# Kernel tuning notes

Hardware: AMD Instinct MI355X
Metric: run time of the kernel (lower is better)

Reference implementation:

```python
import jax, jax.numpy as jnp
import numpy as np

D_MODEL = 1024
NUM_HEADS = 16
D_K = D_MODEL // NUM_HEADS


def setup_inputs() -> dict:
    key = jax.random.key(0)
    ks = jax.random.split(key, 9)
    s = 1.0 / np.sqrt(D_MODEL)
    x = jax.random.normal(ks[0], (4, 2048, D_MODEL), dtype=jnp.float32)
    wq = jax.random.uniform(ks[1], (D_MODEL, D_MODEL), jnp.float32, -s, s)
    bq = jax.random.uniform(ks[2], (D_MODEL,), jnp.float32, -s, s)
    wk = jax.random.uniform(ks[3], (D_MODEL, D_MODEL), jnp.float32, -s, s)
    bk = jax.random.uniform(ks[4], (D_MODEL,), jnp.float32, -s, s)
    wv = jax.random.uniform(ks[5], (D_MODEL, D_MODEL), jnp.float32, -s, s)
    bv = jax.random.uniform(ks[6], (D_MODEL,), jnp.float32, -s, s)
    wo = jax.random.uniform(ks[7], (D_MODEL, D_MODEL), jnp.float32, -s, s)
    bo = jax.random.uniform(ks[8], (D_MODEL,), jnp.float32, -s, s)
    return {"x": x, "wq": wq, "bq": bq, "wk": wk, "bk": bk,
            "wv": wv, "bv": bv, "wo": wo, "bo": bo}


def reference(x, wq, bq, wk, bk, wv, bv, wo, bo):
    B, S, _ = x.shape
    H, Dk = NUM_HEADS, D_K
    # QKV projections (torch Linear: y = x @ W.T + b; here w* stored as [in,out])
    q = (x @ wq + bq).reshape(B, S, H, Dk).transpose(0, 2, 1, 3)  # [B,H,S,Dk]
    k = (x @ wk + bk).reshape(B, S, H, Dk).transpose(0, 2, 1, 3)
    v = (x @ wv + bv).reshape(B, S, H, Dk).transpose(0, 2, 1, 3)
    scores = jnp.einsum('bhqd,bhkd->bhqk', q, k) / jnp.sqrt(jnp.float32(Dk))
    attn = jax.nn.softmax(scores, axis=-1)
    out = jnp.einsum('bhqk,bhkd->bhqd', attn, v)  # [B,H,S,Dk]
    out = out.transpose(0, 2, 1, 3).reshape(B, S, H * Dk)
    return out @ wo + bo
```

## Files before the change

### kernel.cpp

```cpp
#include <hip/hip_runtime.h>
#include <hip/hip_bf16.h>
#include <cstdint>

#define D_MODEL 1024
#define NHEAD 16
#define DKH 64
#define BATCH 4
#define SEQ 2048
#define M_TOT (BATCH*SEQ)

typedef __bf16 bf16;
typedef __bf16 bf16x8 __attribute__((ext_vector_type(8)));
typedef __bf16 bf16x4 __attribute__((ext_vector_type(4)));
typedef float  f32x4  __attribute__((ext_vector_type(4)));

__device__ __forceinline__ void async_ld16(const void* g, void* l) {
    __builtin_amdgcn_global_load_lds(
        (__attribute__((address_space(1))) void*)(uintptr_t)g,
        (__attribute__((address_space(3))) void*)(uintptr_t)l,
        16, 0, 0);
}

__global__ __launch_bounds__(256) void k_cvt(const float* __restrict__ x,
                                             bf16* __restrict__ xb,
                                             const float* __restrict__ wq,
                                             const float* __restrict__ wk,
                                             const float* __restrict__ wv,
                                             const float* __restrict__ wo,
                                             bf16* __restrict__ wt) {
    __shared__ float t[32][33];
    int bid = blockIdx.x;
    if (bid < 8192) {
        int i = (bid * 256 + threadIdx.x) * 4;
        float4 f = *(const float4*)(x + i);
        bf16x4 o;
        o[0] = (bf16)f.x; o[1] = (bf16)f.y; o[2] = (bf16)f.z; o[3] = (bf16)f.w;
        *(bf16x4*)(xb + i) = o;
    } else {
        int wb = bid - 8192;
        int z = wb >> 10;
        int rem = wb & 1023;
        const float* W = (z == 0) ? wq : (z == 1) ? wk : (z == 2) ? wv : wo;
        bf16* T = wt + (size_t)z * D_MODEL * D_MODEL;
        int tx = threadIdx.x & 31, ty = threadIdx.x >> 5;
        int bx = (rem & 31) * 32, by = (rem >> 5) * 32;
#pragma unroll
        for (int i = 0; i < 4; i++)
            t[ty + i * 8][tx] = W[(size_t)(by + ty + i * 8) * D_MODEL + bx + tx];
        __syncthreads();
#pragma unroll
        for (int i = 0; i < 4; i++)
            T[(size_t)(bx + ty + i * 8) * D_MODEL + by + tx] = (bf16)t[tx][ty + i * 8];
    }
}

__global__ __launch_bounds__(256) void k_gemm_qkv(const bf16* __restrict__ xb,
                                                  const bf16* __restrict__ wt,
                                                  const float* __restrict__ bq,
                                                  const float* __restrict__ bk,
                                                  const float* __restrict__ bv,
                                                  bf16* __restrict__ qkv,
                                                  bf16* __restrict__ vtg) {
    __shared__ bf16 As[2 * 128 * 32];
    __shared__ bf16 Bs[2 * 128 * 32];

    int tid = threadIdx.x;
    int lane = tid & 63, wid = tid >> 6;
    int ln = lane & 15, qd = lane >> 4;
    int wm = wid >> 1, wn = wid & 1;
    int m0 = blockIdx.x * 128;
    int n0 = blockIdx.y * 128;
    int z = n0 >> 10;
    const float* bias = (z == 0) ? bq : (z == 1) ? bk : bv;
    float scale = (z == 0) ? 0.125f * 1.44269504088896f : 1.0f;
    bool swapped = (z < 2);

    f32x4 zero4 = {0.f, 0.f, 0.f, 0.f};
    f32x4 acc[4][4];
#pragma unroll
    for (int i = 0; i < 4; i++)
#pragma unroll
        for (int j = 0; j < 4; j++) acc[i][j] = zero4;

    for (int k0 = 0; k0 < D_MODEL; k0 += 64) {
#pragma unroll
        for (int t = 0; t < 4; t++) {
            int c = t * 256 + tid;
            int ch = c >> 9, w = c & 511;
            int row = w >> 2, part = w & 3;
            async_ld16(xb + (size_t)(m0 + row) * D_MODEL + k0 + ch * 32 + part * 8,
                       As + ch * 4096 + (w & ~63) * 8);
            async_ld16(wt + (size_t)(n0 + row) * D_MODEL + k0 + ch * 32 + part * 8,
                       Bs + ch * 4096 + (w & ~63) * 8);
        }
        __syncthreads();
#pragma unroll
        for (int kc = 0; kc < 2; kc++) {
            bf16x8 af[4], bfr[4];
#pragma unroll
            for (int mi = 0; mi < 4; mi++)
                af[mi] = *(const bf16x8*)(As + kc * 4096 + (wm * 64 + mi * 16 + ln) * 32 + qd * 8);
#pragma unroll
            for (int ni = 0; ni < 4; ni++)
                bfr[ni] = *(const bf16x8*)(Bs + kc * 4096 + (wn * 64 + ni * 16 + ln) * 32 + qd * 8);
            if (swapped) {
#pragma unroll
                for (int mi = 0; mi < 4; mi++)
#pragma unroll
                    for (int ni = 0; ni < 4; ni++)
                        acc[mi][ni] = __builtin_amdgcn_mfma_f32_16x16x32_bf16(bfr[ni], af[mi],
                                                                              acc[mi][ni], 0, 0, 0);
            } else {
#pragma unroll
                for (int mi = 0; mi < 4; mi++)
#pragma unroll
                    for (int ni = 0; ni < 4; ni++)
                        acc[mi][ni] = __builtin_amdgcn_mfma_f32_16x16x32_bf16(af[mi], bfr[ni],
                                                                              acc[mi][ni], 0, 0, 0);
            }
        }
        __syncthreads();
    }

    if (swapped) {
        bf16* out = qkv + (size_t)z * M_TOT * D_MODEL;
#pragma unroll
        for (int mi = 0; mi < 4; mi++) {
            int srow = m0 + wm * 64 + mi * 16 + ln;
            int b = srow >> 11, s = srow & 2047;
#pragma unroll
            for (int ni = 0; ni < 4; ni++) {
                int colz = (n0 & 1023) + wn * 64 + ni * 16 + qd * 4;
                f32x4 bb = *(const f32x4*)(bias + colz);
                int h = colz >> 6, d = colz & 63;
                bf16x4 p;
#pragma unroll
                for (int r = 0; r < 4; r++)
                    p[r] = (bf16)((acc[mi][ni][r] + bb[r]) * scale);
                *(bf16x4*)(out + (((size_t)(b * NHEAD + h)) * SEQ + s) * DKH + d) = p;
            }
        }
    } else {
#pragma unroll
        for (int ni = 0; ni < 4; ni++) {
            int colz = (n0 & 1023) + wn * 64 + ni * 16 + ln;
            float bcol = bias[colz];
            int h = colz >> 6, d = colz & 63;
#pragma unroll
            for (int mi = 0; mi < 4; mi++) {
                int rb = m0 + wm * 64 + mi * 16 + qd * 4;
                int b = rb >> 11, s = rb & 2047;
                bf16x4 p;
#pragma unroll
                for (int r = 0; r < 4; r++)
                    p[r] = (bf16)(acc[mi][ni][r] + bcol);
                *(bf16x4*)(vtg + (((size_t)(b * NHEAD + h)) * DKH + d) * SEQ + s) = p;
            }
        }
    }
}

#define PROW 36
__global__ __launch_bounds__(256, 4) void k_attn(const bf16* __restrict__ qg,
                                                 const bf16* __restrict__ kg,
                                                 const bf16* __restrict__ vtg,
                                                 bf16* __restrict__ og) {
    __shared__ bf16 Ks[2 * 64 * 32];
    __shared__ bf16 Vs[2 * 64 * 32];
    __shared__ bf16 Ps[4 * 2 * 32 * PROW];

    int tid = threadIdx.x;
    int lane = tid & 63, wid = tid >> 6;
    int ln = lane & 15, qd = lane >> 4;
    int bh = blockIdx.x;
    int q0 = blockIdx.y * 128;
    int b = bh >> 4, h = bh & 15;

    const bf16* qp = qg + (size_t)bh * SEQ * DKH;
    const bf16* kp = kg + (size_t)bh * SEQ * DKH;
    const bf16* vp = vtg + (size_t)bh * DKH * SEQ;

    bf16x8 qa[2][2];
#pragma unroll
    for (int mi = 0; mi < 2; mi++)
#pragma unroll
        for (int kc = 0; kc < 2; kc++)
            qa[mi][kc] = *(const bf16x8*)(qp + (size_t)(q0 + wid * 32 + mi * 16 + ln) * DKH
                                          + kc * 32 + qd * 8);

    bf16 onev = (bf16)((ln == 0) ? 1.0f : 0.0f);
    bf16x8 ones_frag = {onev, onev, onev, onev, onev, onev, onev, onev};

    f32x4 zero4 = {0.f, 0.f, 0.f, 0.f};
    f32x4 o_acc[2][4];
    f32x4 l_acc[2];
#pragma unroll
    for (int mi = 0; mi < 2; mi++) {
        l_acc[mi] = zero4;
#pragma unroll
        for (int nd = 0; nd < 4; nd++) o_acc[mi][nd] = zero4;
    }

    bf16* Pw = Ps + wid * 2 * 32 * PROW;

    for (int kt = 0; kt < SEQ; kt += 64) {
#pragma unroll
        for (int t = 0; t < 2; t++) {
            int c = t * 256 + tid;
            int ch = c >> 8, w = c & 255;
            int row = w >> 2, part = w & 3;
            async_ld16(kp + (size_t)(kt + row) * DKH + ch * 32 + part * 8,
                       Ks + (c & ~63) * 8);
            async_ld16(vp + (size_t)row * SEQ + kt + ch * 32 + part * 8,
                       Vs + (c & ~63) * 8);
        }
        __syncthreads();

        f32x4 sc[2][4];
#pragma unroll
        for (int mi = 0; mi < 2; mi++)
#pragma unroll
            for (int ni = 0; ni < 4; ni++) sc[mi][ni] = zero4;
#pragma unroll
        for (int kc = 0; kc < 2; kc++) {
#pragma unroll
            for (int ni = 0; ni < 4; ni++) {
                bf16x8 kb = *(const bf16x8*)(Ks + kc * 2048 + (ni * 16 + ln) * 32 + qd * 8);
#pragma unroll
                for (int mi = 0; mi < 2; mi++)
                    sc[mi][ni] = __builtin_amdgcn_mfma_f32_16x16x32_bf16(kb, qa[mi][kc],
                                                                         sc[mi][ni], 0, 0, 0);
            }
        }

#pragma unroll
        for (int mi = 0; mi < 2; mi++) {
#pragma unroll
            for (int ni = 0; ni < 4; ni++) {
                bf16x4 p4;
#pragma unroll
                for (int r = 0; r < 4; r++)
                    p4[r] = (bf16)__builtin_amdgcn_exp2f(sc[mi][ni][r]);
                *(bf16x4*)(Pw + (ni >> 1) * 32 * PROW + (mi * 16 + ln) * PROW
                           + (ni & 1) * 16 + qd * 4) = p4;
            }
        }

#pragma unroll
        for (int kc2 = 0; kc2 < 2; kc2++) {
            bf16x8 pf[2];
#pragma unroll
            for (int mi = 0; mi < 2; mi++) {
                const bf16* pr = Pw + kc2 * 32 * PROW + (mi * 16 + ln) * PROW + qd * 8;
                bf16x4 lo = *(const bf16x4*)(pr);
                bf16x4 hi = *(const bf16x4*)(pr + 4);
                pf[mi][0] = lo[0]; pf[mi][1] = lo[1]; pf[mi][2] = lo[2]; pf[mi][3] = lo[3];
                pf[mi][4] = hi[0]; pf[mi][5] = hi[1]; pf[mi][6] = hi[2]; pf[mi][7] = hi[3];
                l_acc[mi] = __builtin_amdgcn_mfma_f32_16x16x32_bf16(pf[mi], ones_frag,
                                                                    l_acc[mi], 0, 0, 0);
            }
#pragma unroll
            for (int nd = 0; nd < 4; nd++) {
                bf16x8 vf = *(const bf16x8*)(Vs + kc2 * 2048 + (nd * 16 + ln) * 32 + qd * 8);
#pragma unroll
                for (int mi = 0; mi < 2; mi++)
                    o_acc[mi][nd] = __builtin_amdgcn_mfma_f32_16x16x32_bf16(pf[mi], vf,
                                                                            o_acc[mi][nd], 0, 0, 0);
            }
        }
        __syncthreads();
    }

#pragma unroll
    for (int mi = 0; mi < 2; mi++) {
#pragma unroll
        for (int r = 0; r < 4; r++) {
            float lsum = __shfl(l_acc[mi][r], lane & 48, 64);
            float inv = 1.0f / lsum;
            int s = q0 + wid * 32 + mi * 16 + qd * 4 + r;
            size_t rowoff = ((size_t)b * SEQ + s) * D_MODEL + h * DKH;
#pragma unroll
            for (int nd = 0; nd < 4; nd++)
                og[rowoff + nd * 16 + ln] = (bf16)(o_acc[mi][nd][r] * inv);
        }
    }
}

__global__ __launch_bounds__(256) void k_gemm_out(const bf16* __restrict__ ob,
                                                  const bf16* __restrict__ wot,
                                                  const float* __restrict__ bo,
                                                  float* __restrict__ out) {
    __shared__ bf16 As[2 * 128 * 32];
    __shared__ bf16 Bs[2 * 128 * 32];

    int tid = threadIdx.x;
    int lane = tid & 63, wid = tid >> 6;
    int ln = lane & 15, qd = lane >> 4;
    int wm = wid >> 1, wn = wid & 1;
    int m0 = blockIdx.x * 128, n0 = blockIdx.y * 128;

    f32x4 zero4 = {0.f, 0.f, 0.f, 0.f};
    f32x4 acc[4][4];
#pragma unroll
    for (int i = 0; i < 4; i++)
#pragma unroll
        for (int j = 0; j < 4; j++) acc[i][j] = zero4;

    for (int k0 = 0; k0 < D_MODEL; k0 += 64) {
#pragma unroll
        for (int t = 0; t < 4; t++) {
            int c = t * 256 + tid;
            int ch = c >> 9, w = c & 511;
            int row = w >> 2, part = w & 3;
            async_ld16(ob + (size_t)(m0 + row) * D_MODEL + k0 + ch * 32 + part * 8,
                       As + ch * 4096 + (w & ~63) * 8);
            async_ld16(wot + (size_t)(n0 + row) * D_MODEL + k0 + ch * 32 + part * 8,
                       Bs + ch * 4096 + (w & ~63) * 8);
        }
        __syncthreads();
#pragma unroll
        for (int kc = 0; kc < 2; kc++) {
            bf16x8 af[4], bfr[4];
#pragma unroll
            for (int mi = 0; mi < 4; mi++)
                af[mi] = *(const bf16x8*)(As + kc * 4096 + (wm * 64 + mi * 16 + ln) * 32 + qd * 8);
#pragma unroll
            for (int ni = 0; ni < 4; ni++)
                bfr[ni] = *(const bf16x8*)(Bs + kc * 4096 + (wn * 64 + ni * 16 + ln) * 32 + qd * 8);
#pragma unroll
            for (int mi = 0; mi < 4; mi++)
#pragma unroll
                for (int ni = 0; ni < 4; ni++)
                    acc[mi][ni] = __builtin_amdgcn_mfma_f32_16x16x32_bf16(bfr[ni], af[mi],
                                                                          acc[mi][ni], 0, 0, 0);
        }
        __syncthreads();
    }

#pragma unroll
    for (int mi = 0; mi < 4; mi++) {
        int row = m0 + wm * 64 + mi * 16 + ln;
#pragma unroll
        for (int ni = 0; ni < 4; ni++) {
            int col4 = n0 + wn * 64 + ni * 16 + qd * 4;
            f32x4 bb = *(const f32x4*)(bo + col4);
            f32x4 v;
#pragma unroll
            for (int r = 0; r < 4; r++) v[r] = acc[mi][ni][r] + bb[r];
            *(f32x4*)(out + (size_t)row * D_MODEL + col4) = v;
        }
    }
}

extern "C" void kernel_launch(void* const* d_in, const int* in_sizes, int n_in,
                              void* d_out, int out_size, void* d_ws, size_t ws_size,
                              hipStream_t stream) {
    const float* x  = (const float*)d_in[0];
    const float* wq = (const float*)d_in[1];
    const float* bq = (const float*)d_in[2];
    const float* wk = (const float*)d_in[3];
    const float* bk = (const float*)d_in[4];
    const float* wv = (const float*)d_in[5];
    const float* bv = (const float*)d_in[6];
    const float* wo = (const float*)d_in[7];
    const float* bo = (const float*)d_in[8];
    float* out = (float*)d_out;

    char* ws = (char*)d_ws;
    bf16* xb  = (bf16*)ws;
    bf16* wt  = (bf16*)(ws + 16777216);
    bf16* qkv = (bf16*)(ws + 25165824);
    bf16* vtg = (bf16*)(ws + 75497472);
    bf16* og  = xb;

    k_cvt<<<dim3(8192 + 4096), dim3(256), 0, stream>>>(x, xb, wq, wk, wv, wo, wt);
    k_gemm_qkv<<<dim3(64, 24), dim3(256), 0, stream>>>(xb, wt, bq, bk, bv, qkv, vtg);
    k_attn<<<dim3(64, 16), dim3(256), 0, stream>>>(qkv, qkv + (size_t)M_TOT * D_MODEL, vtg, og);
    k_gemm_out<<<dim3(64, 8), dim3(256), 0, stream>>>(og, wt + 3 * (size_t)D_MODEL * D_MODEL,
                                                      bo, out);
}
```

Before: 271.6 us.

## Rewrite attention with 32x32 MFMA, register P, double-buffered swizzled K/V

The attention kernel moves from 16x16x32 to 32x32x16 bf16 MFMAs. The softmax probabilities stay in registers, repacked with v_permlane32_swap, instead of going through an LDS scratch tile, and the row sum is accumulated with plain adds instead of an extra ones-MFMA. K/V tiles are double-buffered with async global-to-LDS loads, so the next tile's fetch overlaps compute, and an XOR swizzle avoids bank conflicts. The cost is more LDS per block and a lower occupancy hint (3 instead of 4 blocks).

```diff
diff --git a/kernel.cpp b/kernel.cpp
--- a/kernel.cpp
+++ b/kernel.cpp
@@ -13,12 +13,19 @@
 typedef __bf16 bf16x8 __attribute__((ext_vector_type(8)));
 typedef __bf16 bf16x4 __attribute__((ext_vector_type(4)));
 typedef float  f32x4  __attribute__((ext_vector_type(4)));
+typedef float  f32x16 __attribute__((ext_vector_type(16)));
 
 __device__ __forceinline__ void async_ld16(const void* g, void* l) {
     __builtin_amdgcn_global_load_lds(
         (__attribute__((address_space(1))) void*)(uintptr_t)g,
         (__attribute__((address_space(3))) void*)(uintptr_t)l,
         16, 0, 0);
+}
+
+__device__ __forceinline__ unsigned pack2_bf16(float lo, float hi) {
+    union { __bf16 h[2]; unsigned u; } w;
+    w.h[0] = (bf16)lo; w.h[1] = (bf16)hi;
+    return w.u;
 }
 
 __global__ __launch_bounds__(256) void k_cvt(const float* __restrict__ x,
@@ -160,18 +167,16 @@
     }
 }
 
-#define PROW 36
-__global__ __launch_bounds__(256, 4) void k_attn(const bf16* __restrict__ qg,
+__global__ __launch_bounds__(256, 3) void k_attn(const bf16* __restrict__ qg,
                                                  const bf16* __restrict__ kg,
                                                  const bf16* __restrict__ vtg,
                                                  bf16* __restrict__ og) {
-    __shared__ bf16 Ks[2 * 64 * 32];
-    __shared__ bf16 Vs[2 * 64 * 32];
-    __shared__ bf16 Ps[4 * 2 * 32 * PROW];
+    __shared__ bf16 Ks[2 * 64 * 64];
+    __shared__ bf16 Vs[2 * 64 * 64];
 
     int tid = threadIdx.x;
     int lane = tid & 63, wid = tid >> 6;
-    int ln = lane & 15, qd = lane >> 4;
+    int ln32 = lane & 31, hi = lane >> 5;
     int bh = blockIdx.x;
     int q0 = blockIdx.y * 128;
     int b = bh >> 4, h = bh & 15;
@@ -180,110 +185,105 @@
     const bf16* kp = kg + (size_t)bh * SEQ * DKH;
     const bf16* vp = vtg + (size_t)bh * DKH * SEQ;
 
-    bf16x8 qa[2][2];
-#pragma unroll
-    for (int mi = 0; mi < 2; mi++)
-#pragma unroll
-        for (int kc = 0; kc < 2; kc++)
-            qa[mi][kc] = *(const bf16x8*)(qp + (size_t)(q0 + wid * 32 + mi * 16 + ln) * DKH
-                                          + kc * 32 + qd * 8);
-
-    bf16 onev = (bf16)((ln == 0) ? 1.0f : 0.0f);
-    bf16x8 ones_frag = {onev, onev, onev, onev, onev, onev, onev, onev};
-
-    f32x4 zero4 = {0.f, 0.f, 0.f, 0.f};
-    f32x4 o_acc[2][4];
-    f32x4 l_acc[2];
-#pragma unroll
-    for (int mi = 0; mi < 2; mi++) {
-        l_acc[mi] = zero4;
-#pragma unroll
-        for (int nd = 0; nd < 4; nd++) o_acc[mi][nd] = zero4;
-    }
-
-    bf16* Pw = Ps + wid * 2 * 32 * PROW;
-
-    for (int kt = 0; kt < SEQ; kt += 64) {
+    auto STAGE = [&](int bb, int kt) {
 #pragma unroll
         for (int t = 0; t < 2; t++) {
             int c = t * 256 + tid;
-            int ch = c >> 8, w = c & 255;
-            int row = w >> 2, part = w & 3;
-            async_ld16(kp + (size_t)(kt + row) * DKH + ch * 32 + part * 8,
-                       Ks + (c & ~63) * 8);
-            async_ld16(vp + (size_t)row * SEQ + kt + ch * 32 + part * 8,
-                       Vs + (c & ~63) * 8);
-        }
-        __syncthreads();
-
-        f32x4 sc[2][4];
-#pragma unroll
-        for (int mi = 0; mi < 2; mi++)
-#pragma unroll
-            for (int ni = 0; ni < 4; ni++) sc[mi][ni] = zero4;
-#pragma unroll
-        for (int kc = 0; kc < 2; kc++) {
-#pragma unroll
-            for (int ni = 0; ni < 4; ni++) {
-                bf16x8 kb = *(const bf16x8*)(Ks + kc * 2048 + (ni * 16 + ln) * 32 + qd * 8);
-#pragma unroll
-                for (int mi = 0; mi < 2; mi++)
-                    sc[mi][ni] = __builtin_amdgcn_mfma_f32_16x16x32_bf16(kb, qa[mi][kc],
-                                                                         sc[mi][ni], 0, 0, 0);
-            }
-        }
-
-#pragma unroll
-        for (int mi = 0; mi < 2; mi++) {
-#pragma unroll
-            for (int ni = 0; ni < 4; ni++) {
-                bf16x4 p4;
-#pragma unroll
-                for (int r = 0; r < 4; r++)
-                    p4[r] = (bf16)__builtin_amdgcn_exp2f(sc[mi][ni][r]);
-                *(bf16x4*)(Pw + (ni >> 1) * 32 * PROW + (mi * 16 + ln) * PROW
-                           + (ni & 1) * 16 + qd * 4) = p4;
-            }
-        }
-
-#pragma unroll
-        for (int kc2 = 0; kc2 < 2; kc2++) {
-            bf16x8 pf[2];
-#pragma unroll
-            for (int mi = 0; mi < 2; mi++) {
-                const bf16* pr = Pw + kc2 * 32 * PROW + (mi * 16 + ln) * PROW + qd * 8;
-                bf16x4 lo = *(const bf16x4*)(pr);
-                bf16x4 hi = *(const bf16x4*)(pr + 4);
-                pf[mi][0] = lo[0]; pf[mi][1] = lo[1]; pf[mi][2] = lo[2]; pf[mi][3] = lo[3];
-                pf[mi][4] = hi[0]; pf[mi][5] = hi[1]; pf[mi][6] = hi[2]; pf[mi][7] = hi[3];
-                l_acc[mi] = __builtin_amdgcn_mfma_f32_16x16x32_bf16(pf[mi], ones_frag,
-                                                                    l_acc[mi], 0, 0, 0);
-            }
-#pragma unroll
-            for (int nd = 0; nd < 4; nd++) {
-                bf16x8 vf = *(const bf16x8*)(Vs + kc2 * 2048 + (nd * 16 + ln) * 32 + qd * 8);
-#pragma unroll
-                for (int mi = 0; mi < 2; mi++)
-                    o_acc[mi][nd] = __builtin_amdgcn_mfma_f32_16x16x32_bf16(pf[mi], vf,
-                                                                            o_acc[mi][nd], 0, 0, 0);
-            }
-        }
-        __syncthreads();
-    }
-
-#pragma unroll
-    for (int mi = 0; mi < 2; mi++) {
-#pragma unroll
-        for (int r = 0; r < 4; r++) {
-            float lsum = __shfl(l_acc[mi][r], lane & 48, 64);
-            float inv = 1.0f / lsum;
-            int s = q0 + wid * 32 + mi * 16 + qd * 4 + r;
-            size_t rowoff = ((size_t)b * SEQ + s) * D_MODEL + h * DKH;
-#pragma unroll
-            for (int nd = 0; nd < 4; nd++)
-                og[rowoff + nd * 16 + ln] = (bf16)(o_acc[mi][nd][r] * inv);
-        }
-    }
+            int row = c >> 3, chl = c & 7;
+            int chg = chl ^ ((row ^ (row >> 3)) & 7);
+            async_ld16(kp + (size_t)(kt + row) * DKH + chg * 8,
+                       Ks + bb * 4096 + (c & ~63) * 8);
+            async_ld16(vp + (size_t)row * SEQ + kt + chg * 8,
+                       Vs + bb * 4096 + (c & ~63) * 8);
+        }
+    };
+
+    STAGE(0, 0);
+
+    bf16x8 qa[4];
+#pragma unroll
+    for (int kk = 0; kk < 4; kk++)
+        qa[kk] = *(const bf16x8*)(qp + (size_t)(q0 + wid * 32 + ln32) * DKH + kk * 16 + hi * 8);
+
+    f32x16 o_acc[2];
+#pragma unroll
+    for (int db = 0; db < 2; db++)
+#pragma unroll
+        for (int r = 0; r < 16; r++) o_acc[db][r] = 0.f;
+    f32x4 lsum4 = {0.f, 0.f, 0.f, 0.f};
+
+    asm volatile("s_waitcnt vmcnt(0)" ::: "memory");
+    __builtin_amdgcn_s_barrier();
+
+    for (int t = 0; t < 32; t++) {
+        int bb = t & 1;
+        if (t < 31) STAGE(bb ^ 1, (t + 1) * 64);
+
+        f32x16 sc[2];
+#pragma unroll
+        for (int kb = 0; kb < 2; kb++)
+#pragma unroll
+            for (int r = 0; r < 16; r++) sc[kb][r] = 0.f;
+#pragma unroll
+        for (int kk = 0; kk < 4; kk++) {
+#pragma unroll
+            for (int kb = 0; kb < 2; kb++) {
+                int kr = kb * 32 + ln32;
+                bf16x8 kf = *(const bf16x8*)(Ks + bb * 4096 + kr * 64
+                                + (size_t)(((2 * kk + hi) ^ ((kr ^ (kr >> 3)) & 7)) * 8));
+                sc[kb] = __builtin_amdgcn_mfma_f32_32x32x16_bf16(kf, qa[kk], sc[kb], 0, 0, 0);
+            }
+        }
+
+#pragma unroll
+        for (int kb = 0; kb < 2; kb++) {
+            float e[16];
+#pragma unroll
+            for (int r = 0; r < 16; r++) e[r] = __builtin_amdgcn_exp2f(sc[kb][r]);
+#pragma unroll
+            for (int r = 0; r < 16; r++) lsum4[r & 3] += e[r];
+            unsigned pd[8];
+#pragma unroll
+            for (int j = 0; j < 8; j++) pd[j] = pack2_bf16(e[2 * j], e[2 * j + 1]);
+#pragma unroll
+            for (int ks = 0; ks < 2; ks++) {
+                unsigned a0 = pd[ks * 4 + 0], b0 = pd[ks * 4 + 2];
+                unsigned a1 = pd[ks * 4 + 1], b1 = pd[ks * 4 + 3];
+                asm volatile("v_permlane32_swap_b32 %0, %1" : "+v"(a0), "+v"(b0));
+                asm volatile("v_permlane32_swap_b32 %0, %1" : "+v"(a1), "+v"(b1));
+                union { unsigned u[4]; bf16x8 v; } pf;
+                pf.u[0] = a0; pf.u[1] = a1; pf.u[2] = b0; pf.u[3] = b1;
+#pragma unroll
+                for (int db = 0; db < 2; db++) {
+                    int vr = db * 32 + ln32;
+                    bf16x8 vf = *(const bf16x8*)(Vs + bb * 4096 + vr * 64
+                                    + (size_t)(((4 * kb + 2 * ks + hi) ^ ((vr ^ (vr >> 3)) & 7)) * 8));
+                    o_acc[db] = __builtin_amdgcn_mfma_f32_32x32x16_bf16(vf, pf.v, o_acc[db], 0, 0, 0);
+                }
+            }
+        }
+
+        if (t < 31) {
+            asm volatile("s_waitcnt vmcnt(0)" ::: "memory");
+            __builtin_amdgcn_s_barrier();
+        }
+    }
+
+    float lsum = (lsum4[0] + lsum4[1]) + (lsum4[2] + lsum4[3]);
+    float lt = lsum + __shfl_xor(lsum, 32, 64);
+    float inv = 1.0f / lt;
+
+    int s = q0 + wid * 32 + ln32;
+    size_t rowoff = ((size_t)b * SEQ + s) * D_MODEL + h * DKH;
+#pragma unroll
+    for (int db = 0; db < 2; db++)
+#pragma unroll
+        for (int q4 = 0; q4 < 4; q4++) {
+            bf16x4 pv4;
+#pragma unroll
+            for (int j = 0; j < 4; j++) pv4[j] = (bf16)(o_acc[db][q4 * 4 + j] * inv);
+            *(bf16x4*)(og + rowoff + db * 32 + q4 * 8 + hi * 4) = pv4;
+        }
 }
 
 __global__ __launch_bounds__(256) void k_gemm_out(const bf16* __restrict__ ob,
```

Measured after the change: 290.8 us. +7.1%, slower.

## Triple-buffer GEMM LDS staging with async prefetch and XOR-swizzled layout

Applied to the files above, without the earlier changes.

Both projection GEMMs (QKV and output) drop the single-stage load, sync, compute, sync loop over 64-wide K chunks. They now use a three-slot ring of 32-wide K tiles, with async global-to-LDS loads issued two steps ahead and partial vmcnt waits, so each step needs one barrier instead of two. LDS chunks are XOR-swizzled by row to cut bank conflicts on the fragment reads. The cost is more LDS per block (48KB), which may lower occupancy, plus reliance on hand-written vmcnt counts being correct.

```diff
diff --git a/kernel.cpp b/kernel.cpp
--- a/kernel.cpp
+++ b/kernel.cpp
@@ -54,6 +54,7 @@
     }
 }
 
+
 __global__ __launch_bounds__(256) void k_gemm_qkv(const bf16* __restrict__ xb,
                                                   const bf16* __restrict__ wt,
                                                   const float* __restrict__ bq,
@@ -61,8 +62,7 @@
                                                   const float* __restrict__ bv,
                                                   bf16* __restrict__ qkv,
                                                   bf16* __restrict__ vtg) {
-    __shared__ bf16 As[2 * 128 * 32];
-    __shared__ bf16 Bs[2 * 128 * 32];
+    __shared__ bf16 S[6 * 4096];
 
     int tid = threadIdx.x;
     int lane = tid & 63, wid = tid >> 6;
@@ -75,6 +75,20 @@
     float scale = (z == 0) ? 0.125f * 1.44269504088896f : 1.0f;
     bool swapped = (z < 2);
 
+    const bf16* Ag = xb + (size_t)m0 * D_MODEL;
+    const bf16* Bg = wt + (size_t)n0 * D_MODEL;
+
+    auto STAGEU = [&](const bf16* gbase, int k0, int slot) {
+#pragma unroll
+        for (int i = 0; i < 2; i++) {
+            int c = i * 256 + tid;
+            int row = c >> 2, chl = c & 3;
+            int chg = chl ^ ((row ^ (row >> 2)) & 3);
+            async_ld16(gbase + (size_t)row * D_MODEL + k0 + chg * 8,
+                       S + slot * 4096 + (c & ~63) * 8);
+        }
+    };
+
     f32x4 zero4 = {0.f, 0.f, 0.f, 0.f};
     f32x4 acc[4][4];
 #pragma unroll
@@ -82,44 +96,83 @@
 #pragma unroll
         for (int j = 0; j < 4; j++) acc[i][j] = zero4;
 
-    for (int k0 = 0; k0 < D_MODEL; k0 += 64) {
-#pragma unroll
-        for (int t = 0; t < 4; t++) {
-            int c = t * 256 + tid;
-            int ch = c >> 9, w = c & 511;
-            int row = w >> 2, part = w & 3;
-            async_ld16(xb + (size_t)(m0 + row) * D_MODEL + k0 + ch * 32 + part * 8,
-                       As + ch * 4096 + (w & ~63) * 8);
-            async_ld16(wt + (size_t)(n0 + row) * D_MODEL + k0 + ch * 32 + part * 8,
-                       Bs + ch * 4096 + (w & ~63) * 8);
-        }
-        __syncthreads();
-#pragma unroll
-        for (int kc = 0; kc < 2; kc++) {
-            bf16x8 af[4], bfr[4];
+    unsigned aoff[4], boff[4];
+#pragma unroll
+    for (int mi = 0; mi < 4; mi++) {
+        int row = wm * 64 + mi * 16 + ln;
+        aoff[mi] = (unsigned)(row * 32 + ((qd ^ ((row ^ (row >> 2)) & 3)) * 8));
+    }
+#pragma unroll
+    for (int ni = 0; ni < 4; ni++) {
+        int row = wn * 64 + ni * 16 + ln;
+        boff[ni] = (unsigned)(row * 32 + ((qd ^ ((row ^ (row >> 2)) & 3)) * 8));
+    }
+
+    STAGEU(Ag, 0, 0);  STAGEU(Bg, 0, 1);
+    STAGEU(Ag, 32, 2); STAGEU(Bg, 32, 3);
+
+    const int NSTEP = D_MODEL / 32;
+    int ca = 0;
+    int cp = 2;
+    for (int t = 0; t < NSTEP - 1; t++) {
+        asm volatile("s_waitcnt vmcnt(4)" ::: "memory");
+        __builtin_amdgcn_s_barrier();
+        asm volatile("" ::: "memory");
+        if (t < NSTEP - 2) {
+            STAGEU(Ag, (t + 2) * 32, 2 * cp);
+            STAGEU(Bg, (t + 2) * 32, 2 * cp + 1);
+        }
+        bf16x8 af[4], bfr[4];
+#pragma unroll
+        for (int mi = 0; mi < 4; mi++)
+            af[mi] = *(const bf16x8*)(S + (2 * ca) * 4096 + aoff[mi]);
+#pragma unroll
+        for (int ni = 0; ni < 4; ni++)
+            bfr[ni] = *(const bf16x8*)(S + (2 * ca + 1) * 4096 + boff[ni]);
+        if (swapped) {
 #pragma unroll
             for (int mi = 0; mi < 4; mi++)
-                af[mi] = *(const bf16x8*)(As + kc * 4096 + (wm * 64 + mi * 16 + ln) * 32 + qd * 8);
-#pragma unroll
-            for (int ni = 0; ni < 4; ni++)
-                bfr[ni] = *(const bf16x8*)(Bs + kc * 4096 + (wn * 64 + ni * 16 + ln) * 32 + qd * 8);
-            if (swapped) {
-#pragma unroll
-                for (int mi = 0; mi < 4; mi++)
-#pragma unroll
-                    for (int ni = 0; ni < 4; ni++)
-                        acc[mi][ni] = __builtin_amdgcn_mfma_f32_16x16x32_bf16(bfr[ni], af[mi],
-                                                                              acc[mi][ni], 0, 0, 0);
-            } else {
-#pragma unroll
-                for (int mi = 0; mi < 4; mi++)
-#pragma unroll
-                    for (int ni = 0; ni < 4; ni++)
-                        acc[mi][ni] = __builtin_amdgcn_mfma_f32_16x16x32_bf16(af[mi], bfr[ni],
-                                                                              acc[mi][ni], 0, 0, 0);
-            }
-        }
-        __syncthreads();
+#pragma unroll
+                for (int ni = 0; ni < 4; ni++)
+                    acc[mi][ni] = __builtin_amdgcn_mfma_f32_16x16x32_bf16(bfr[ni], af[mi],
+                                                                          acc[mi][ni], 0, 0, 0);
+        } else {
+#pragma unroll
+            for (int mi = 0; mi < 4; mi++)
+#pragma unroll
+                for (int ni = 0; ni < 4; ni++)
+                    acc[mi][ni] = __builtin_amdgcn_mfma_f32_16x16x32_bf16(af[mi], bfr[ni],
+                                                                          acc[mi][ni], 0, 0, 0);
+        }
+        ca = (ca == 2) ? 0 : ca + 1;
+        cp = (cp == 2) ? 0 : cp + 1;
+    }
+    {
+        asm volatile("s_waitcnt vmcnt(0)" ::: "memory");
+        __builtin_amdgcn_s_barrier();
+        asm volatile("" ::: "memory");
+        bf16x8 af[4], bfr[4];
+#pragma unroll
+        for (int mi = 0; mi < 4; mi++)
+            af[mi] = *(const bf16x8*)(S + (2 * ca) * 4096 + aoff[mi]);
+#pragma unroll
+        for (int ni = 0; ni < 4; ni++)
+            bfr[ni] = *(const bf16x8*)(S + (2 * ca + 1) * 4096 + boff[ni]);
+        if (swapped) {
+#pragma unroll
+            for (int mi = 0; mi < 4; mi++)
+#pragma unroll
+                for (int ni = 0; ni < 4; ni++)
+                    acc[mi][ni] = __builtin_amdgcn_mfma_f32_16x16x32_bf16(bfr[ni], af[mi],
+                                                                          acc[mi][ni], 0, 0, 0);
+        } else {
+#pragma unroll
+            for (int mi = 0; mi < 4; mi++)
+#pragma unroll
+                for (int ni = 0; ni < 4; ni++)
+                    acc[mi][ni] = __builtin_amdgcn_mfma_f32_16x16x32_bf16(af[mi], bfr[ni],
+                                                                          acc[mi][ni], 0, 0, 0);
+        }
     }
 
     if (swapped) {
@@ -290,8 +343,7 @@
                                                   const bf16* __restrict__ wot,
                                                   const float* __restrict__ bo,
                                                   float* __restrict__ out) {
-    __shared__ bf16 As[2 * 128 * 32];
-    __shared__ bf16 Bs[2 * 128 * 32];
+    __shared__ bf16 S[6 * 4096];
 
     int tid = threadIdx.x;
     int lane = tid & 63, wid = tid >> 6;
@@ -299,6 +351,20 @@
     int wm = wid >> 1, wn = wid & 1;
     int m0 = blockIdx.x * 128, n0 = blockIdx.y * 128;
 
+    const bf16* Ag = ob + (size_t)m0 * D_MODEL;
+    const bf16* Bg = wot + (size_t)n0 * D_MODEL;
+
+    auto STAGEU = [&](const bf16* gbase, int k0, int slot) {
+#pragma unroll
+        for (int i = 0; i < 2; i++) {
+            int c = i * 256 + tid;
+            int row = c >> 2, chl = c & 3;
+            int chg = chl ^ ((row ^ (row >> 2)) & 3);
+            async_ld16(gbase + (size_t)row * D_MODEL + k0 + chg * 8,
+                       S + slot * 4096 + (c & ~63) * 8);
+        }
+    };
+
     f32x4 zero4 = {0.f, 0.f, 0.f, 0.f};
     f32x4 acc[4][4];
 #pragma unroll
@@ -306,35 +372,64 @@
 #pragma unroll
         for (int j = 0; j < 4; j++) acc[i][j] = zero4;
 
-    for (int k0 = 0; k0 < D_MODEL; k0 += 64) {
-#pragma unroll
-        for (int t = 0; t < 4; t++) {
-            int c = t * 256 + tid;
-            int ch = c >> 9, w = c & 511;
-            int row = w >> 2, part = w & 3;
-            async_ld16(ob + (size_t)(m0 + row) * D_MODEL + k0 + ch * 32 + part * 8,
-                       As + ch * 4096 + (w & ~63) * 8);
-            async_ld16(wot + (size_t)(n0 + row) * D_MODEL + k0 + ch * 32 + part * 8,
-                       Bs + ch * 4096 + (w & ~63) * 8);
-        }
-        __syncthreads();
-#pragma unroll
-        for (int kc = 0; kc < 2; kc++) {
-            bf16x8 af[4], bfr[4];
-#pragma unroll
-            for (int mi = 0; mi < 4; mi++)
-                af[mi] = *(const bf16x8*)(As + kc * 4096 + (wm * 64 + mi * 16 + ln) * 32 + qd * 8);
+    unsigned aoff[4], boff[4];
+#pragma unroll
+    for (int mi = 0; mi < 4; mi++) {
+        int row = wm * 64 + mi * 16 + ln;
+        aoff[mi] = (unsigned)(row * 32 + ((qd ^ ((row ^ (row >> 2)) & 3)) * 8));
+    }
+#pragma unroll
+    for (int ni = 0; ni < 4; ni++) {
+        int row = wn * 64 + ni * 16 + ln;
+        boff[ni] = (unsigned)(row * 32 + ((qd ^ ((row ^ (row >> 2)) & 3)) * 8));
+    }
+
+    STAGEU(Ag, 0, 0);  STAGEU(Bg, 0, 1);
+    STAGEU(Ag, 32, 2); STAGEU(Bg, 32, 3);
+
+    const int NSTEP = D_MODEL / 32;
+    int ca = 0, cp = 2;
+    for (int t = 0; t < NSTEP - 1; t++) {
+        asm volatile("s_waitcnt vmcnt(4)" ::: "memory");
+        __builtin_amdgcn_s_barrier();
+        asm volatile("" ::: "memory");
+        if (t < NSTEP - 2) {
+            STAGEU(Ag, (t + 2) * 32, 2 * cp);
+            STAGEU(Bg, (t + 2) * 32, 2 * cp + 1);
+        }
+        bf16x8 af[4], bfr[4];
+#pragma unroll
+        for (int mi = 0; mi < 4; mi++)
+            af[mi] = *(const bf16x8*)(S + (2 * ca) * 4096 + aoff[mi]);
+#pragma unroll
+        for (int ni = 0; ni < 4; ni++)
+            bfr[ni] = *(const bf16x8*)(S + (2 * ca + 1) * 4096 + boff[ni]);
+#pragma unroll
+        for (int mi = 0; mi < 4; mi++)
 #pragma unroll
             for (int ni = 0; ni < 4; ni++)
-                bfr[ni] = *(const bf16x8*)(Bs + kc * 4096 + (wn * 64 + ni * 16 + ln) * 32 + qd * 8);
-#pragma unroll
-            for (int mi = 0; mi < 4; mi++)
-#pragma unroll
-                for (int ni = 0; ni < 4; ni++)
-                    acc[mi][ni] = __builtin_amdgcn_mfma_f32_16x16x32_bf16(bfr[ni], af[mi],
-                                                                          acc[mi][ni], 0, 0, 0);
-        }
-        __syncthreads();
+                acc[mi][ni] = __builtin_amdgcn_mfma_f32_16x16x32_bf16(bfr[ni], af[mi],
+                                                                      acc[mi][ni], 0, 0, 0);
+        ca = (ca == 2) ? 0 : ca + 1;
+        cp = (cp == 2) ? 0 : cp + 1;
+    }
+    {
+        asm volatile("s_waitcnt vmcnt(0)" ::: "memory");
+        __builtin_amdgcn_s_barrier();
+        asm volatile("" ::: "memory");
+        bf16x8 af[4], bfr[4];
+#pragma unroll
+        for (int mi = 0; mi < 4; mi++)
+            af[mi] = *(const bf16x8*)(S + (2 * ca) * 4096 + aoff[mi]);
+#pragma unroll
+        for (int ni = 0; ni < 4; ni++)
+            bfr[ni] = *(const bf16x8*)(S + (2 * ca + 1) * 4096 + boff[ni]);
+#pragma unroll
+        for (int mi = 0; mi < 4; mi++)
+#pragma unroll
+            for (int ni = 0; ni < 4; ni++)
+                acc[mi][ni] = __builtin_amdgcn_mfma_f32_16x16x32_bf16(bfr[ni], af[mi],
+                                                                      acc[mi][ni], 0, 0, 0);
     }
 
 #pragma unroll
```

Result: slower. 281.6 us (+3.7%).

## Enlarge QKV GEMM tile to 256x256 with double-buffered async LDS pipeline

Applied to the files above, without the earlier changes.

The QKV projection GEMM now uses 512-thread blocks computing 256x256 output tiles, with 8 waves each holding an 8x4 grid of MFMA accumulators. Global-to-LDS async loads for the next K slice are issued mid-iteration into a second buffer, coordinated through manual vmcnt waits and raw barriers, and MFMA sections are wrapped in s_setprio. The aim is to cut global traffic per FLOP and hide load latency behind compute. In exchange it uses more registers and LDS per block and launches only 384 blocks, which may leave some CUs underused.

```diff
diff --git a/kernel.cpp b/kernel.cpp
--- a/kernel.cpp
+++ b/kernel.cpp
@@ -54,79 +54,122 @@
     }
 }
 
-__global__ __launch_bounds__(256) void k_gemm_qkv(const bf16* __restrict__ xb,
+__global__ __launch_bounds__(512) void k_gemm_qkv(const bf16* __restrict__ xb,
                                                   const bf16* __restrict__ wt,
                                                   const float* __restrict__ bq,
                                                   const float* __restrict__ bk,
                                                   const float* __restrict__ bv,
                                                   bf16* __restrict__ qkv,
                                                   bf16* __restrict__ vtg) {
-    __shared__ bf16 As[2 * 128 * 32];
-    __shared__ bf16 Bs[2 * 128 * 32];
+    __shared__ bf16 As[2 * 16384];
+    __shared__ bf16 Bs[2 * 16384];
 
     int tid = threadIdx.x;
     int lane = tid & 63, wid = tid >> 6;
     int ln = lane & 15, qd = lane >> 4;
-    int wm = wid >> 1, wn = wid & 1;
-    int m0 = blockIdx.x * 128;
-    int n0 = blockIdx.y * 128;
+    int wm = wid >> 2, wn = wid & 3;
+    int m0 = blockIdx.x * 256;
+    int n0 = blockIdx.y * 256;
     int z = n0 >> 10;
     const float* bias = (z == 0) ? bq : (z == 1) ? bk : bv;
     float scale = (z == 0) ? 0.125f * 1.44269504088896f : 1.0f;
     bool swapped = (z < 2);
 
+    int c0 = tid, c1 = tid + 512;
+    const bf16* agA0 = xb + (size_t)(m0 + (c0 >> 2)) * D_MODEL + (c0 & 3) * 8;
+    const bf16* agA1 = xb + (size_t)(m0 + (c1 >> 2)) * D_MODEL + (c1 & 3) * 8;
+    const bf16* bgB0 = wt + (size_t)(n0 + (c0 >> 2)) * D_MODEL + (c0 & 3) * 8;
+    const bf16* bgB1 = wt + (size_t)(n0 + (c1 >> 2)) * D_MODEL + (c1 & 3) * 8;
+    bf16* ldA0 = As + (c0 & ~63) * 8;
+    bf16* ldA1 = As + (c1 & ~63) * 8;
+    bf16* ldB0 = Bs + (c0 & ~63) * 8;
+    bf16* ldB1 = Bs + (c1 & ~63) * 8;
+
+    auto SA = [&](int off, int gk) {
+        async_ld16(agA0 + gk, ldA0 + off);
+        async_ld16(agA1 + gk, ldA1 + off);
+    };
+    auto SB = [&](int off, int gk) {
+        async_ld16(bgB0 + gk, ldB0 + off);
+        async_ld16(bgB1 + gk, ldB1 + off);
+    };
+
+    unsigned aro = (unsigned)((wm * 128 + ln) * 32 + qd * 8);
+    unsigned bro = (unsigned)((wn * 64 + ln) * 32 + qd * 8);
+
     f32x4 zero4 = {0.f, 0.f, 0.f, 0.f};
-    f32x4 acc[4][4];
-#pragma unroll
-    for (int i = 0; i < 4; i++)
+    f32x4 acc[8][4];
+#pragma unroll
+    for (int i = 0; i < 8; i++)
 #pragma unroll
         for (int j = 0; j < 4; j++) acc[i][j] = zero4;
 
-    for (int k0 = 0; k0 < D_MODEL; k0 += 64) {
-#pragma unroll
-        for (int t = 0; t < 4; t++) {
-            int c = t * 256 + tid;
-            int ch = c >> 9, w = c & 511;
-            int row = w >> 2, part = w & 3;
-            async_ld16(xb + (size_t)(m0 + row) * D_MODEL + k0 + ch * 32 + part * 8,
-                       As + ch * 4096 + (w & ~63) * 8);
-            async_ld16(wt + (size_t)(n0 + row) * D_MODEL + k0 + ch * 32 + part * 8,
-                       Bs + ch * 4096 + (w & ~63) * 8);
-        }
-        __syncthreads();
-#pragma unroll
-        for (int kc = 0; kc < 2; kc++) {
-            bf16x8 af[4], bfr[4];
-#pragma unroll
-            for (int mi = 0; mi < 4; mi++)
-                af[mi] = *(const bf16x8*)(As + kc * 4096 + (wm * 64 + mi * 16 + ln) * 32 + qd * 8);
-#pragma unroll
-            for (int ni = 0; ni < 4; ni++)
-                bfr[ni] = *(const bf16x8*)(Bs + kc * 4096 + (wn * 64 + ni * 16 + ln) * 32 + qd * 8);
-            if (swapped) {
-#pragma unroll
-                for (int mi = 0; mi < 4; mi++)
-#pragma unroll
-                    for (int ni = 0; ni < 4; ni++)
-                        acc[mi][ni] = __builtin_amdgcn_mfma_f32_16x16x32_bf16(bfr[ni], af[mi],
-                                                                              acc[mi][ni], 0, 0, 0);
-            } else {
-#pragma unroll
-                for (int mi = 0; mi < 4; mi++)
-#pragma unroll
-                    for (int ni = 0; ni < 4; ni++)
-                        acc[mi][ni] = __builtin_amdgcn_mfma_f32_16x16x32_bf16(af[mi], bfr[ni],
-                                                                              acc[mi][ni], 0, 0, 0);
-            }
-        }
-        __syncthreads();
+    auto PP = [&](int co, int kh, int so, int sg, int gk, int wait4) {
+        if (wait4) asm volatile("s_waitcnt vmcnt(4)" ::: "memory");
+        else       asm volatile("s_waitcnt vmcnt(0)" ::: "memory");
+        __builtin_amdgcn_s_barrier();
+        asm volatile("" ::: "memory");
+        if (sg) SA(so + kh, gk);
+        bf16x8 af[8], b0, b1, b2, b3;
+#pragma unroll
+        for (int mi = 0; mi < 8; mi++)
+            af[mi] = *(const bf16x8*)(As + co + kh + aro + mi * 512);
+        b0 = *(const bf16x8*)(Bs + co + kh + bro);
+        b1 = *(const bf16x8*)(Bs + co + kh + bro + 512);
+        __builtin_amdgcn_s_setprio(1);
+        if (swapped) {
+#pragma unroll
+            for (int mi = 0; mi < 8; mi++) {
+                acc[mi][0] = __builtin_amdgcn_mfma_f32_16x16x32_bf16(b0, af[mi], acc[mi][0], 0, 0, 0);
+                acc[mi][1] = __builtin_amdgcn_mfma_f32_16x16x32_bf16(b1, af[mi], acc[mi][1], 0, 0, 0);
+            }
+        } else {
+#pragma unroll
+            for (int mi = 0; mi < 8; mi++) {
+                acc[mi][0] = __builtin_amdgcn_mfma_f32_16x16x32_bf16(af[mi], b0, acc[mi][0], 0, 0, 0);
+                acc[mi][1] = __builtin_amdgcn_mfma_f32_16x16x32_bf16(af[mi], b1, acc[mi][1], 0, 0, 0);
+            }
+        }
+        __builtin_amdgcn_s_setprio(0);
+        if (sg) SB(so + kh, gk);
+        b2 = *(const bf16x8*)(Bs + co + kh + bro + 1024);
+        b3 = *(const bf16x8*)(Bs + co + kh + bro + 1536);
+        __builtin_amdgcn_s_setprio(1);
+        if (swapped) {
+#pragma unroll
+            for (int mi = 0; mi < 8; mi++) {
+                acc[mi][2] = __builtin_amdgcn_mfma_f32_16x16x32_bf16(b2, af[mi], acc[mi][2], 0, 0, 0);
+                acc[mi][3] = __builtin_amdgcn_mfma_f32_16x16x32_bf16(b3, af[mi], acc[mi][3], 0, 0, 0);
+            }
+        } else {
+#pragma unroll
+            for (int mi = 0; mi < 8; mi++) {
+                acc[mi][2] = __builtin_amdgcn_mfma_f32_16x16x32_bf16(af[mi], b2, acc[mi][2], 0, 0, 0);
+                acc[mi][3] = __builtin_amdgcn_mfma_f32_16x16x32_bf16(af[mi], b3, acc[mi][3], 0, 0, 0);
+            }
+        }
+        __builtin_amdgcn_s_setprio(0);
+    };
+
+    SA(0, 0); SB(0, 0); SA(8192, 32); SB(8192, 32);
+
+    for (int t = 0; t < 15; t++) {
+        int co = (t & 1) * 16384;
+        int so = co ^ 16384;
+        int kn = (t + 1) * 64;
+        PP(co, 0,    so, 1, kn,      1);
+        PP(co, 8192, so, 1, kn + 32, 1);
+    }
+    {
+        PP(16384, 0,    0, 0, 0, 1);
+        PP(16384, 8192, 0, 0, 0, 0);
     }
 
     if (swapped) {
         bf16* out = qkv + (size_t)z * M_TOT * D_MODEL;
 #pragma unroll
-        for (int mi = 0; mi < 4; mi++) {
-            int srow = m0 + wm * 64 + mi * 16 + ln;
+        for (int mi = 0; mi < 8; mi++) {
+            int srow = m0 + wm * 128 + mi * 16 + ln;
             int b = srow >> 11, s = srow & 2047;
 #pragma unroll
             for (int ni = 0; ni < 4; ni++) {
@@ -147,8 +190,8 @@
             float bcol = bias[colz];
             int h = colz >> 6, d = colz & 63;
 #pragma unroll
-            for (int mi = 0; mi < 4; mi++) {
-                int rb = m0 + wm * 64 + mi * 16 + qd * 4;
+            for (int mi = 0; mi < 8; mi++) {
+                int rb = m0 + wm * 128 + mi * 16 + qd * 4;
                 int b = rb >> 11, s = rb & 2047;
                 bf16x4 p;
 #pragma unroll
@@ -374,7 +417,7 @@
     bf16* og  = xb;
 
     k_cvt<<<dim3(8192 + 4096), dim3(256), 0, stream>>>(x, xb, wq, wk, wv, wo, wt);
-    k_gemm_qkv<<<dim3(64, 24), dim3(256), 0, stream>>>(xb, wt, bq, bk, bv, qkv, vtg);
+    k_gemm_qkv<<<dim3(32, 12), dim3(512), 0, stream>>>(xb, wt, bq, bk, bv, qkv, vtg);
     k_attn<<<dim3(64, 16), dim3(256), 0, stream>>>(qkv, qkv + (size_t)M_TOT * D_MODEL, vtg, og);
     k_gemm_out<<<dim3(64, 8), dim3(256), 0, stream>>>(og, wt + 3 * (size_t)D_MODEL * D_MODEL,
                                                       bo, out);
```

Result: slower. 549.6 us (+102.4%).
